# Kernel optimization log

Hardware: AMD Instinct MI355X
Metric: run time of the kernel (lower is better)

Reference implementation:

```python
import jax, jax.numpy as jnp
import numpy as np


def setup_inputs() -> dict:
    key = jax.random.key(0)
    # (B, C, H, W) with H == W, required by the original module's broadcasting.
    x = jax.random.normal(key, (16, 64, 256, 256), dtype=jnp.float32)
    return {"x": x}


def reference(x):
    """Naive real DFT of the original module, computed as a separable contraction.

    Original math (after resolving the meshgrid 'xy' indexing, H == W == N):
      real[b,c,u,v] = sum_{i,j} x[b,c,i,j] * cos(2*pi*(j*u + i*v)/N)
      imag[b,c,u,v] = sum_{i,j} x[b,c,i,j] * sin(-2*pi*(j*u + i*v)/N)
    with u in [0, N/2), v in [0, N/2).
    We use cos(a+b)=cos a cos b - sin a sin b to factorize into matmuls,
    avoiding the (B,C,N,N,N/2,N/2) broadcast intermediate.
    """
    B, C, H, W = x.shape
    assert H == W, "original module's broadcasting requires square input"
    N = H
    K = N // 2
    two_pi = jnp.asarray(2.0 * np.pi, dtype=x.dtype)
    n = jnp.arange(N, dtype=x.dtype) / N          # spatial index / N
    k = jnp.arange(K, dtype=x.dtype)              # frequency index
    ang = two_pi * n[:, None] * k[None, :]        # (N, K)
    Cm = jnp.cos(ang)                             # (N, K)
    Sm = jnp.sin(ang)                             # (N, K)

    # Contract W-axis j against frequency u, then H-axis i against frequency v.
    A = jnp.einsum('bcij,ju->bciu', x, Cm)        # sum_j x * cos(2pi j u / N)
    Bt = jnp.einsum('bcij,ju->bciu', x, Sm)       # sum_j x * sin(2pi j u / N)
    real = jnp.einsum('bciu,iv->bcuv', A, Cm) - jnp.einsum('bciu,iv->bcuv', Bt, Sm)
    imag = -(jnp.einsum('bciu,iv->bcuv', Bt, Cm) + jnp.einsum('bciu,iv->bcuv', A, Sm))
    return real, imag
```

## Files before the change

### kernel.cpp

```cpp
#include <hip/hip_runtime.h>
#include <hip/hip_bf16.h>


typedef __attribute__((ext_vector_type(8))) short short8;
typedef __attribute__((ext_vector_type(4))) short bf16x4;
typedef __attribute__((ext_vector_type(4))) float f32x4;

#define NN 256
#define KF 128
#define NIMG 1024

__device__ __align__(16) short g_Ct[KF * NN];
__device__ __align__(16) short g_St[KF * NN];
__device__ __align__(16) short g_Stn[KF * NN];

__device__ __forceinline__ short f2bf(float f) {
    union { float f; unsigned u; } v; v.f = f;
    unsigned r = v.u + 0x7FFFu + ((v.u >> 16) & 1u);
    return (short)(r >> 16);
}

__global__ void gen_tables() {
    int tid = blockIdx.x * blockDim.x + threadIdx.x;
    if (tid >= KF * NN) return;
    int u = tid >> 8;
    int j = tid & 255;
    int phase = (u * j) & 255;
    float ang = (float)phase * 0.02454369260617026f;
    float s, c;
    sincosf(ang, &s, &c);
    g_Ct[tid]  = f2bf(c);
    g_St[tid]  = f2bf(s);
    g_Stn[tid] = f2bf(-s);
}

#define MFMA(a, b, c) __builtin_amdgcn_mfma_f32_16x16x32_bf16(a, b, c, 0, 0, 0)

__global__ __launch_bounds__(512, 4) void freq_dft(const float* __restrict__ x,
                                                   float* __restrict__ out) {
    __shared__ __align__(16) char lds[65536];

    const int bid = blockIdx.x;
    const int cc  = bid & 7;
    const int q   = bid >> 3;
    const int h   = q & 1;
    const int img = cc + ((q >> 1) << 3);

    const float* __restrict__ X = x + (size_t)img * (NN * NN);
    float* __restrict__ outR = out + (size_t)img * (KF * KF);
    float* __restrict__ outI = outR + (size_t)NIMG * (KF * KF);

    const int lane = threadIdx.x & 63;
    const int wave = threadIdx.x >> 6;
    const int l15  = lane & 15;
    const int lk8  = (lane >> 4) << 3;
    const int lr4  = (lane >> 4) << 2;

    {
        const short* __restrict__ srcC = g_Ct  + h * 64 * NN;
        const short* __restrict__ srcS = g_Stn + h * 64 * NN;
        #pragma unroll
        for (int k = 0; k < 4; ++k) {
            int slot = threadIdx.x + k * 512;
            int row  = slot >> 5;
            int chk  = slot & 31;
            int byte = row * 512 + ((chk << 4) ^ ((row & 7) << 4));
            short8 vC = *(const short8*)(srcC + row * NN + chk * 8);
            short8 vS = *(const short8*)(srcS + row * NN + chk * 8);
            *(short8*)(lds + byte)         = vC;
            *(short8*)(lds + 32768 + byte) = vS;
        }
    }
    __syncthreads();

    f32x4 accA[2][4], accB[2][4];
    {
        const int i0 = wave * 32;
        #pragma unroll
        for (int fi = 0; fi < 2; ++fi)
            #pragma unroll
            for (int fu = 0; fu < 4; ++fu) {
                accA[fi][fu] = (f32x4){0.f, 0.f, 0.f, 0.f};
                accB[fi][fu] = (f32x4){0.f, 0.f, 0.f, 0.f};
            }
        const float* __restrict__ xp0 = X + (i0 + l15) * NN + lk8;
        const float* __restrict__ xp1 = X + (i0 + 16 + l15) * NN + lk8;
        const int wst = wave;
        const int jA  = (wst & 7) * 32;
        const int jB  = ((wst + 1) & 7) * 32;
        f32x4 a0 = *(const f32x4*)(xp0 + jA), a1 = *(const f32x4*)(xp0 + jA + 4);
        f32x4 a2 = *(const f32x4*)(xp1 + jA), a3 = *(const f32x4*)(xp1 + jA + 4);
        f32x4 b0 = *(const f32x4*)(xp0 + jB), b1 = *(const f32x4*)(xp0 + jB + 4);
        f32x4 b2 = *(const f32x4*)(xp1 + jB), b3 = *(const f32x4*)(xp1 + jB + 4);
        #pragma unroll
        for (int t = 0; t < 8; ++t) {
            const int j0 = ((t + wst) & 7) * 32;
            f32x4 c0 = a0, c1 = a1, c2 = a2, c3 = a3;
            a0 = b0; a1 = b1; a2 = b2; a3 = b3;
            if (t < 6) {
                const int jn = ((t + 2 + wst) & 7) * 32;
                b0 = *(const f32x4*)(xp0 + jn); b1 = *(const f32x4*)(xp0 + jn + 4);
                b2 = *(const f32x4*)(xp1 + jn); b3 = *(const f32x4*)(xp1 + jn + 4);
            }
            short8 xb0, xb1;
            xb0[0] = f2bf(c0[0]); xb0[1] = f2bf(c0[1]); xb0[2] = f2bf(c0[2]); xb0[3] = f2bf(c0[3]);
            xb0[4] = f2bf(c1[0]); xb0[5] = f2bf(c1[1]); xb0[6] = f2bf(c1[2]); xb0[7] = f2bf(c1[3]);
            xb1[0] = f2bf(c2[0]); xb1[1] = f2bf(c2[1]); xb1[2] = f2bf(c2[2]); xb1[3] = f2bf(c2[3]);
            xb1[4] = f2bf(c3[0]); xb1[5] = f2bf(c3[1]); xb1[6] = f2bf(c3[2]); xb1[7] = f2bf(c3[3]);
            short8 ca[4], sa[4];
            #pragma unroll
            for (int fu = 0; fu < 4; ++fu) {
                int row  = fu * 16 + l15;
                int byte = row * 512 + (((j0 + lk8) * 2) ^ ((row & 7) << 4));
                ca[fu] = *(const short8*)(lds + byte);
                sa[fu] = *(const short8*)(lds + 32768 + byte);
            }
            #pragma unroll
            for (int fu = 0; fu < 4; ++fu) {
                accA[0][fu] = MFMA(xb0, ca[fu], accA[0][fu]);
                accA[1][fu] = MFMA(xb1, ca[fu], accA[1][fu]);
                accB[0][fu] = MFMA(xb0, sa[fu], accB[0][fu]);
                accB[1][fu] = MFMA(xb1, sa[fu], accB[1][fu]);
            }
        }
    }
    __syncthreads();

    {
        const int i0 = wave * 32;
        #pragma unroll
        for (int fi = 0; fi < 2; ++fi)
            #pragma unroll
            for (int fu = 0; fu < 4; ++fu) {
                int ul    = fu * 16 + l15;
                int ibase = i0 + fi * 16 + lr4;
                int byte  = ul * 512 + ((ibase * 2) ^ ((ul & 7) << 4));
                bf16x4 a4, b4;
                #pragma unroll
                for (int r = 0; r < 4; ++r) {
                    a4[r] = f2bf(accA[fi][fu][r]);
                    b4[r] = f2bf(accB[fi][fu][r]);
                }
                *(bf16x4*)(lds + byte)         = a4;
                *(bf16x4*)(lds + 32768 + byte) = b4;
            }
    }
    __syncthreads();

    {
        const int wu = wave >> 2;
        const int wv = wave & 3;
        const short8 smask = {(short)0x8000, (short)0x8000, (short)0x8000, (short)0x8000,
                              (short)0x8000, (short)0x8000, (short)0x8000, (short)0x8000};
        f32x4 accR[2][2], accI[2][2];
        #pragma unroll
        for (int fu = 0; fu < 2; ++fu)
            #pragma unroll
            for (int fv = 0; fv < 2; ++fv) {
                accR[fu][fv] = (f32x4){0.f, 0.f, 0.f, 0.f};
                accI[fu][fv] = (f32x4){0.f, 0.f, 0.f, 0.f};
            }
        const short* __restrict__ tC0 = g_Ct + (wv * 32 + l15) * NN + lk8;
        const short* __restrict__ tC1 = g_Ct + (wv * 32 + 16 + l15) * NN + lk8;
        const short* __restrict__ tS0 = g_St + (wv * 32 + l15) * NN + lk8;
        const short* __restrict__ tS1 = g_St + (wv * 32 + 16 + l15) * NN + lk8;
        const int wst = wave;
        const int iA  = (wst & 7) * 32;
        const int iB  = ((wst + 1) & 7) * 32;
        short8 ac0 = *(const short8*)(tC0 + iA), ac1 = *(const short8*)(tC1 + iA);
        short8 as0 = *(const short8*)(tS0 + iA), as1 = *(const short8*)(tS1 + iA);
        short8 bc0 = *(const short8*)(tC0 + iB), bc1 = *(const short8*)(tC1 + iB);
        short8 bs0 = *(const short8*)(tS0 + iB), bs1 = *(const short8*)(tS1 + iB);
        #pragma unroll
        for (int t = 0; t < 8; ++t) {
            const int is = ((t + wst) & 7) * 32;
            short8 cb0 = ac0, cb1 = ac1, sb0 = as0, sb1 = as1;
            ac0 = bc0; ac1 = bc1; as0 = bs0; as1 = bs1;
            if (t < 6) {
                const int in = ((t + 2 + wst) & 7) * 32;
                bc0 = *(const short8*)(tC0 + in); bc1 = *(const short8*)(tC1 + in);
                bs0 = *(const short8*)(tS0 + in); bs1 = *(const short8*)(tS1 + in);
            }
            short8 nb0 = sb0 ^ smask;
            short8 nb1 = sb1 ^ smask;
            short8 a[2], bn[2];
            #pragma unroll
            for (int fu = 0; fu < 2; ++fu) {
                int ul   = wu * 32 + fu * 16 + l15;
                int byte = ul * 512 + (((is + lk8) * 2) ^ ((ul & 7) << 4));
                a[fu]  = *(const short8*)(lds + byte);
                bn[fu] = *(const short8*)(lds + 32768 + byte);
            }
            accR[0][0] = MFMA(a[0],  cb0, accR[0][0]);
            accR[1][0] = MFMA(a[1],  cb0, accR[1][0]);
            accR[0][1] = MFMA(a[0],  cb1, accR[0][1]);
            accR[1][1] = MFMA(a[1],  cb1, accR[1][1]);
            accI[0][0] = MFMA(bn[0], cb0, accI[0][0]);
            accI[1][0] = MFMA(bn[1], cb0, accI[1][0]);
            accI[0][1] = MFMA(bn[0], cb1, accI[0][1]);
            accI[1][1] = MFMA(bn[1], cb1, accI[1][1]);
            accR[0][0] = MFMA(bn[0], sb0, accR[0][0]);
            accR[1][0] = MFMA(bn[1], sb0, accR[1][0]);
            accR[0][1] = MFMA(bn[0], sb1, accR[0][1]);
            accR[1][1] = MFMA(bn[1], sb1, accR[1][1]);
            accI[0][0] = MFMA(a[0],  nb0, accI[0][0]);
            accI[1][0] = MFMA(a[1],  nb0, accI[1][0]);
            accI[0][1] = MFMA(a[0],  nb1, accI[0][1]);
            accI[1][1] = MFMA(a[1],  nb1, accI[1][1]);
        }
        #pragma unroll
        for (int fu = 0; fu < 2; ++fu)
            #pragma unroll
            for (int fv = 0; fv < 2; ++fv)
                #pragma unroll
                for (int r = 0; r < 4; ++r) {
                    int u = h * 64 + wu * 32 + fu * 16 + lr4 + r;
                    int v = wv * 32 + fv * 16 + l15;
                    outR[u * KF + v] = accR[fu][fv][r];
                    outI[u * KF + v] = accI[fu][fv][r];
                }
    }
}

extern "C" void kernel_launch(void* const* d_in, const int* in_sizes, int n_in,
                              void* d_out, int out_size, void* d_ws, size_t ws_size,
                              hipStream_t stream) {
    const float* x = (const float*)d_in[0];
    float* out = (float*)d_out;
    gen_tables<<<dim3((KF * NN + 255) / 256), dim3(256), 0, stream>>>();
    freq_dft<<<dim3(NIMG * 2), dim3(512), 0, stream>>>(x, out);
}
```

Measured before the change: 160.7 us.

## Process whole image per block and stream first-stage twiddles from global

Each block now handles one full image instead of half, so the input image is read once rather than twice and the first-stage row transform is no longer duplicated. The first-stage cosine/sine tables are loaded straight from global (L2-resident) into registers with one-step prefetch, instead of being staged through LDS, which drops the initial LDS fill and its barrier. The intermediate needs 128KB of dynamic LDS, so occupancy falls to one block per CU, the launch bound is relaxed, and there is half as many blocks, which risks less latency hiding.

```diff
diff --git a/kernel.cpp b/kernel.cpp
--- a/kernel.cpp
+++ b/kernel.cpp
@@ -36,16 +36,11 @@
 
 #define MFMA(a, b, c) __builtin_amdgcn_mfma_f32_16x16x32_bf16(a, b, c, 0, 0, 0)
 
-__global__ __launch_bounds__(512, 4) void freq_dft(const float* __restrict__ x,
+__global__ __launch_bounds__(512, 2) void freq_dft(const float* __restrict__ x,
                                                    float* __restrict__ out) {
-    __shared__ __align__(16) char lds[65536];
-
-    const int bid = blockIdx.x;
-    const int cc  = bid & 7;
-    const int q   = bid >> 3;
-    const int h   = q & 1;
-    const int img = cc + ((q >> 1) << 3);
-
+    extern __shared__ __align__(16) char lds[];
+
+    const int img = blockIdx.x;
     const float* __restrict__ X = x + (size_t)img * (NN * NN);
     float* __restrict__ outR = out + (size_t)img * (KF * KF);
     float* __restrict__ outI = outR + (size_t)NIMG * (KF * KF);
@@ -55,27 +50,24 @@
     const int l15  = lane & 15;
     const int lk8  = (lane >> 4) << 3;
     const int lr4  = (lane >> 4) << 2;
-
-    {
-        const short* __restrict__ srcC = g_Ct  + h * 64 * NN;
-        const short* __restrict__ srcS = g_Stn + h * 64 * NN;
-        #pragma unroll
-        for (int k = 0; k < 4; ++k) {
-            int slot = threadIdx.x + k * 512;
-            int row  = slot >> 5;
-            int chk  = slot & 31;
-            int byte = row * 512 + ((chk << 4) ^ ((row & 7) << 4));
-            short8 vC = *(const short8*)(srcC + row * NN + chk * 8);
-            short8 vS = *(const short8*)(srcS + row * NN + chk * 8);
-            *(short8*)(lds + byte)         = vC;
-            *(short8*)(lds + 32768 + byte) = vS;
-        }
-    }
-    __syncthreads();
-
-    f32x4 accA[2][4], accB[2][4];
-    {
-        const int i0 = wave * 32;
+    const int wst  = wave;
+
+    const int i0 = wave * 32;
+    const float* __restrict__ xp0 = X + (i0 + l15) * NN + lk8;
+    const float* __restrict__ xp1 = X + (i0 + 16 + l15) * NN + lk8;
+
+    #pragma unroll 1
+    for (int uh = 0; uh < 2; ++uh) {
+        const short* __restrict__ tc0 = g_Ct  + (uh * 64 +  0 + l15) * NN + lk8;
+        const short* __restrict__ tc1 = g_Ct  + (uh * 64 + 16 + l15) * NN + lk8;
+        const short* __restrict__ tc2 = g_Ct  + (uh * 64 + 32 + l15) * NN + lk8;
+        const short* __restrict__ tc3 = g_Ct  + (uh * 64 + 48 + l15) * NN + lk8;
+        const short* __restrict__ ts0 = g_Stn + (uh * 64 +  0 + l15) * NN + lk8;
+        const short* __restrict__ ts1 = g_Stn + (uh * 64 + 16 + l15) * NN + lk8;
+        const short* __restrict__ ts2 = g_Stn + (uh * 64 + 32 + l15) * NN + lk8;
+        const short* __restrict__ ts3 = g_Stn + (uh * 64 + 48 + l15) * NN + lk8;
+
+        f32x4 accA[2][4], accB[2][4];
         #pragma unroll
         for (int fi = 0; fi < 2; ++fi)
             #pragma unroll
@@ -83,18 +75,20 @@
                 accA[fi][fu] = (f32x4){0.f, 0.f, 0.f, 0.f};
                 accB[fi][fu] = (f32x4){0.f, 0.f, 0.f, 0.f};
             }
-        const float* __restrict__ xp0 = X + (i0 + l15) * NN + lk8;
-        const float* __restrict__ xp1 = X + (i0 + 16 + l15) * NN + lk8;
-        const int wst = wave;
-        const int jA  = (wst & 7) * 32;
-        const int jB  = ((wst + 1) & 7) * 32;
+
+        const int jA = (wst & 7) * 32;
+        const int jB = ((wst + 1) & 7) * 32;
         f32x4 a0 = *(const f32x4*)(xp0 + jA), a1 = *(const f32x4*)(xp0 + jA + 4);
         f32x4 a2 = *(const f32x4*)(xp1 + jA), a3 = *(const f32x4*)(xp1 + jA + 4);
         f32x4 b0 = *(const f32x4*)(xp0 + jB), b1 = *(const f32x4*)(xp0 + jB + 4);
         f32x4 b2 = *(const f32x4*)(xp1 + jB), b3 = *(const f32x4*)(xp1 + jB + 4);
+        short8 ca0 = *(const short8*)(tc0 + jA), ca1 = *(const short8*)(tc1 + jA);
+        short8 ca2 = *(const short8*)(tc2 + jA), ca3 = *(const short8*)(tc3 + jA);
+        short8 sa0 = *(const short8*)(ts0 + jA), sa1 = *(const short8*)(ts1 + jA);
+        short8 sa2 = *(const short8*)(ts2 + jA), sa3 = *(const short8*)(ts3 + jA);
+
         #pragma unroll
         for (int t = 0; t < 8; ++t) {
-            const int j0 = ((t + wst) & 7) * 32;
             f32x4 c0 = a0, c1 = a1, c2 = a2, c3 = a3;
             a0 = b0; a1 = b1; a2 = b2; a3 = b3;
             if (t < 6) {
@@ -102,37 +96,40 @@
                 b0 = *(const f32x4*)(xp0 + jn); b1 = *(const f32x4*)(xp0 + jn + 4);
                 b2 = *(const f32x4*)(xp1 + jn); b3 = *(const f32x4*)(xp1 + jn + 4);
             }
+            short8 nc0, nc1, nc2, nc3, ns0, ns1, ns2, ns3;
+            if (t < 7) {
+                const int j1 = ((t + 1 + wst) & 7) * 32;
+                nc0 = *(const short8*)(tc0 + j1); nc1 = *(const short8*)(tc1 + j1);
+                nc2 = *(const short8*)(tc2 + j1); nc3 = *(const short8*)(tc3 + j1);
+                ns0 = *(const short8*)(ts0 + j1); ns1 = *(const short8*)(ts1 + j1);
+                ns2 = *(const short8*)(ts2 + j1); ns3 = *(const short8*)(ts3 + j1);
+            }
             short8 xb0, xb1;
             xb0[0] = f2bf(c0[0]); xb0[1] = f2bf(c0[1]); xb0[2] = f2bf(c0[2]); xb0[3] = f2bf(c0[3]);
             xb0[4] = f2bf(c1[0]); xb0[5] = f2bf(c1[1]); xb0[6] = f2bf(c1[2]); xb0[7] = f2bf(c1[3]);
             xb1[0] = f2bf(c2[0]); xb1[1] = f2bf(c2[1]); xb1[2] = f2bf(c2[2]); xb1[3] = f2bf(c2[3]);
             xb1[4] = f2bf(c3[0]); xb1[5] = f2bf(c3[1]); xb1[6] = f2bf(c3[2]); xb1[7] = f2bf(c3[3]);
-            short8 ca[4], sa[4];
+
+            accA[0][0] = MFMA(xb0, ca0, accA[0][0]); accA[1][0] = MFMA(xb1, ca0, accA[1][0]);
+            accB[0][0] = MFMA(xb0, sa0, accB[0][0]); accB[1][0] = MFMA(xb1, sa0, accB[1][0]);
+            accA[0][1] = MFMA(xb0, ca1, accA[0][1]); accA[1][1] = MFMA(xb1, ca1, accA[1][1]);
+            accB[0][1] = MFMA(xb0, sa1, accB[0][1]); accB[1][1] = MFMA(xb1, sa1, accB[1][1]);
+            accA[0][2] = MFMA(xb0, ca2, accA[0][2]); accA[1][2] = MFMA(xb1, ca2, accA[1][2]);
+            accB[0][2] = MFMA(xb0, sa2, accB[0][2]); accB[1][2] = MFMA(xb1, sa2, accB[1][2]);
+            accA[0][3] = MFMA(xb0, ca3, accA[0][3]); accA[1][3] = MFMA(xb1, ca3, accA[1][3]);
+            accB[0][3] = MFMA(xb0, sa3, accB[0][3]); accB[1][3] = MFMA(xb1, sa3, accB[1][3]);
+
+            if (t < 7) {
+                ca0 = nc0; ca1 = nc1; ca2 = nc2; ca3 = nc3;
+                sa0 = ns0; sa1 = ns1; sa2 = ns2; sa3 = ns3;
+            }
+        }
+
+        #pragma unroll
+        for (int fi = 0; fi < 2; ++fi)
             #pragma unroll
             for (int fu = 0; fu < 4; ++fu) {
-                int row  = fu * 16 + l15;
-                int byte = row * 512 + (((j0 + lk8) * 2) ^ ((row & 7) << 4));
-                ca[fu] = *(const short8*)(lds + byte);
-                sa[fu] = *(const short8*)(lds + 32768 + byte);
-            }
-            #pragma unroll
-            for (int fu = 0; fu < 4; ++fu) {
-                accA[0][fu] = MFMA(xb0, ca[fu], accA[0][fu]);
-                accA[1][fu] = MFMA(xb1, ca[fu], accA[1][fu]);
-                accB[0][fu] = MFMA(xb0, sa[fu], accB[0][fu]);
-                accB[1][fu] = MFMA(xb1, sa[fu], accB[1][fu]);
-            }
-        }
-    }
-    __syncthreads();
-
-    {
-        const int i0 = wave * 32;
-        #pragma unroll
-        for (int fi = 0; fi < 2; ++fi)
-            #pragma unroll
-            for (int fu = 0; fu < 4; ++fu) {
-                int ul    = fu * 16 + l15;
+                int ul    = uh * 64 + fu * 16 + l15;
                 int ibase = i0 + fi * 16 + lr4;
                 int byte  = ul * 512 + ((ibase * 2) ^ ((ul & 7) << 4));
                 bf16x4 a4, b4;
@@ -142,16 +139,22 @@
                     b4[r] = f2bf(accB[fi][fu][r]);
                 }
                 *(bf16x4*)(lds + byte)         = a4;
-                *(bf16x4*)(lds + 32768 + byte) = b4;
+                *(bf16x4*)(lds + 65536 + byte) = b4;
             }
     }
     __syncthreads();
 
-    {
-        const int wu = wave >> 2;
-        const int wv = wave & 3;
-        const short8 smask = {(short)0x8000, (short)0x8000, (short)0x8000, (short)0x8000,
-                              (short)0x8000, (short)0x8000, (short)0x8000, (short)0x8000};
+    const short8 smask = {(short)0x8000, (short)0x8000, (short)0x8000, (short)0x8000,
+                          (short)0x8000, (short)0x8000, (short)0x8000, (short)0x8000};
+    const int vt = wave & 3;
+    const short* __restrict__ tC0 = g_Ct + (vt * 32 +  0 + l15) * NN + lk8;
+    const short* __restrict__ tC1 = g_Ct + (vt * 32 + 16 + l15) * NN + lk8;
+    const short* __restrict__ tS0 = g_St + (vt * 32 +  0 + l15) * NN + lk8;
+    const short* __restrict__ tS1 = g_St + (vt * 32 + 16 + l15) * NN + lk8;
+
+    #pragma unroll 1
+    for (int p = 0; p < 2; ++p) {
+        const int ut = p * 2 + (wave >> 2);
         f32x4 accR[2][2], accI[2][2];
         #pragma unroll
         for (int fu = 0; fu < 2; ++fu)
@@ -160,17 +163,13 @@
                 accR[fu][fv] = (f32x4){0.f, 0.f, 0.f, 0.f};
                 accI[fu][fv] = (f32x4){0.f, 0.f, 0.f, 0.f};
             }
-        const short* __restrict__ tC0 = g_Ct + (wv * 32 + l15) * NN + lk8;
-        const short* __restrict__ tC1 = g_Ct + (wv * 32 + 16 + l15) * NN + lk8;
-        const short* __restrict__ tS0 = g_St + (wv * 32 + l15) * NN + lk8;
-        const short* __restrict__ tS1 = g_St + (wv * 32 + 16 + l15) * NN + lk8;
-        const int wst = wave;
-        const int iA  = (wst & 7) * 32;
-        const int iB  = ((wst + 1) & 7) * 32;
+        const int iA = (wst & 7) * 32;
+        const int iB = ((wst + 1) & 7) * 32;
         short8 ac0 = *(const short8*)(tC0 + iA), ac1 = *(const short8*)(tC1 + iA);
         short8 as0 = *(const short8*)(tS0 + iA), as1 = *(const short8*)(tS1 + iA);
         short8 bc0 = *(const short8*)(tC0 + iB), bc1 = *(const short8*)(tC1 + iB);
         short8 bs0 = *(const short8*)(tS0 + iB), bs1 = *(const short8*)(tS1 + iB);
+
         #pragma unroll
         for (int t = 0; t < 8; ++t) {
             const int is = ((t + wst) & 7) * 32;
@@ -186,10 +185,10 @@
             short8 a[2], bn[2];
             #pragma unroll
             for (int fu = 0; fu < 2; ++fu) {
-                int ul   = wu * 32 + fu * 16 + l15;
+                int ul   = ut * 32 + fu * 16 + l15;
                 int byte = ul * 512 + (((is + lk8) * 2) ^ ((ul & 7) << 4));
                 a[fu]  = *(const short8*)(lds + byte);
-                bn[fu] = *(const short8*)(lds + 32768 + byte);
+                bn[fu] = *(const short8*)(lds + 65536 + byte);
             }
             accR[0][0] = MFMA(a[0],  cb0, accR[0][0]);
             accR[1][0] = MFMA(a[1],  cb0, accR[1][0]);
@@ -214,8 +213,8 @@
             for (int fv = 0; fv < 2; ++fv)
                 #pragma unroll
                 for (int r = 0; r < 4; ++r) {
-                    int u = h * 64 + wu * 32 + fu * 16 + lr4 + r;
-                    int v = wv * 32 + fv * 16 + l15;
+                    int u = ut * 32 + fu * 16 + lr4 + r;
+                    int v = vt * 32 + fv * 16 + l15;
                     outR[u * KF + v] = accR[fu][fv][r];
                     outI[u * KF + v] = accI[fu][fv][r];
                 }
@@ -227,6 +226,8 @@
                               hipStream_t stream) {
     const float* x = (const float*)d_in[0];
     float* out = (float*)d_out;
+    hipFuncSetAttribute((const void*)freq_dft,
+                        hipFuncAttributeMaxDynamicSharedMemorySize, 131072);
     gen_tables<<<dim3((KF * NN + 255) / 256), dim3(256), 0, stream>>>();
-    freq_dft<<<dim3(NIMG * 2), dim3(512), 0, stream>>>(x, out);
-}
+    freq_dft<<<dim3(NIMG), dim3(512), 131072, stream>>>(x, out);
+}
```

After: 226.5 us. 41.0% more time.

## Fold rows i and i+128 into even/odd sums to halve second-stage DFT work

Applied to the files above, without the earlier changes.

The first stage now pairs rows i and i+128 in each wave. Their partial products are combined into sum and difference terms, which serve the even and odd output frequencies because of the period-N symmetry. The second-stage contraction therefore runs over 128 instead of 256 inputs, using new half-size even/odd twiddle tables, and writes adjacent v pairs as float2. Scalar bf16 rounding is also replaced with packed v_cvt_pk_bf16_f32 instructions. The aims are to cut second-stage MFMA and LDS work roughly in half and to reduce conversion ALU cost, at the price of extra tables and slightly different rounding, since the add and subtract happen before the bf16 conversion.

```diff
diff --git a/kernel.cpp b/kernel.cpp
--- a/kernel.cpp
+++ b/kernel.cpp
@@ -5,14 +5,21 @@
 typedef __attribute__((ext_vector_type(8))) short short8;
 typedef __attribute__((ext_vector_type(4))) short bf16x4;
 typedef __attribute__((ext_vector_type(4))) float f32x4;
+typedef __attribute__((ext_vector_type(2))) float f32x2;
+
+typedef union { short8 s8; unsigned u[4]; } pk8;
+typedef union { bf16x4 s4; unsigned u[2]; } pk4;
 
 #define NN 256
 #define KF 128
 #define NIMG 1024
 
 __device__ __align__(16) short g_Ct[KF * NN];
-__device__ __align__(16) short g_St[KF * NN];
 __device__ __align__(16) short g_Stn[KF * NN];
+__device__ __align__(16) short g_T2cE[64 * 128];
+__device__ __align__(16) short g_T2cO[64 * 128];
+__device__ __align__(16) short g_T2sE[64 * 128];
+__device__ __align__(16) short g_T2sO[64 * 128];
 
 __device__ __forceinline__ short f2bf(float f) {
     union { float f; unsigned u; } v; v.f = f;
@@ -20,18 +27,37 @@
     return (short)(r >> 16);
 }
 
+__device__ __forceinline__ unsigned cvtpk(float lo, float hi) {
+    unsigned r;
+    asm("v_cvt_pk_bf16_f32 %0, %1, %2" : "=v"(r) : "v"(lo), "v"(hi));
+    return r;
+}
+
 __global__ void gen_tables() {
     int tid = blockIdx.x * blockDim.x + threadIdx.x;
-    if (tid >= KF * NN) return;
-    int u = tid >> 8;
-    int j = tid & 255;
-    int phase = (u * j) & 255;
-    float ang = (float)phase * 0.02454369260617026f;
-    float s, c;
-    sincosf(ang, &s, &c);
-    g_Ct[tid]  = f2bf(c);
-    g_St[tid]  = f2bf(s);
-    g_Stn[tid] = f2bf(-s);
+    const float w = 0.02454369260617026f;
+    if (tid < KF * NN) {
+        int u = tid >> 8;
+        int j = tid & 255;
+        int phase = (u * j) & 255;
+        float s, c;
+        sincosf((float)phase * w, &s, &c);
+        g_Ct[tid]  = f2bf(c);
+        g_Stn[tid] = f2bf(-s);
+    }
+    if (tid < 64 * 128) {
+        int s = tid >> 7;
+        int i = tid & 127;
+        int pe = (i * (2 * s)) & 255;
+        int po = (i * (2 * s + 1)) & 255;
+        float se, ce, so, co;
+        sincosf((float)pe * w, &se, &ce);
+        sincosf((float)po * w, &so, &co);
+        g_T2cE[tid] = f2bf(ce);
+        g_T2cO[tid] = f2bf(co);
+        g_T2sE[tid] = f2bf(se);
+        g_T2sO[tid] = f2bf(so);
+    }
 }
 
 #define MFMA(a, b, c) __builtin_amdgcn_mfma_f32_16x16x32_bf16(a, b, c, 0, 0, 0)
@@ -55,6 +81,7 @@
     const int l15  = lane & 15;
     const int lk8  = (lane >> 4) << 3;
     const int lr4  = (lane >> 4) << 2;
+    const int wst  = wave;
 
     {
         const short* __restrict__ srcC = g_Ct  + h * 64 * NN;
@@ -75,7 +102,7 @@
 
     f32x4 accA[2][4], accB[2][4];
     {
-        const int i0 = wave * 32;
+        const int i0 = wave * 16;
         #pragma unroll
         for (int fi = 0; fi < 2; ++fi)
             #pragma unroll
@@ -84,10 +111,9 @@
                 accB[fi][fu] = (f32x4){0.f, 0.f, 0.f, 0.f};
             }
         const float* __restrict__ xp0 = X + (i0 + l15) * NN + lk8;
-        const float* __restrict__ xp1 = X + (i0 + 16 + l15) * NN + lk8;
-        const int wst = wave;
-        const int jA  = (wst & 7) * 32;
-        const int jB  = ((wst + 1) & 7) * 32;
+        const float* __restrict__ xp1 = X + (i0 + 128 + l15) * NN + lk8;
+        const int jA = (wst & 7) * 32;
+        const int jB = ((wst + 1) & 7) * 32;
         f32x4 a0 = *(const f32x4*)(xp0 + jA), a1 = *(const f32x4*)(xp0 + jA + 4);
         f32x4 a2 = *(const f32x4*)(xp1 + jA), a3 = *(const f32x4*)(xp1 + jA + 4);
         f32x4 b0 = *(const f32x4*)(xp0 + jB), b1 = *(const f32x4*)(xp0 + jB + 4);
@@ -102,11 +128,13 @@
                 b0 = *(const f32x4*)(xp0 + jn); b1 = *(const f32x4*)(xp0 + jn + 4);
                 b2 = *(const f32x4*)(xp1 + jn); b3 = *(const f32x4*)(xp1 + jn + 4);
             }
-            short8 xb0, xb1;
-            xb0[0] = f2bf(c0[0]); xb0[1] = f2bf(c0[1]); xb0[2] = f2bf(c0[2]); xb0[3] = f2bf(c0[3]);
-            xb0[4] = f2bf(c1[0]); xb0[5] = f2bf(c1[1]); xb0[6] = f2bf(c1[2]); xb0[7] = f2bf(c1[3]);
-            xb1[0] = f2bf(c2[0]); xb1[1] = f2bf(c2[1]); xb1[2] = f2bf(c2[2]); xb1[3] = f2bf(c2[3]);
-            xb1[4] = f2bf(c3[0]); xb1[5] = f2bf(c3[1]); xb1[6] = f2bf(c3[2]); xb1[7] = f2bf(c3[3]);
+            pk8 x0u, x1u;
+            x0u.u[0] = cvtpk(c0[0], c0[1]); x0u.u[1] = cvtpk(c0[2], c0[3]);
+            x0u.u[2] = cvtpk(c1[0], c1[1]); x0u.u[3] = cvtpk(c1[2], c1[3]);
+            x1u.u[0] = cvtpk(c2[0], c2[1]); x1u.u[1] = cvtpk(c2[2], c2[3]);
+            x1u.u[2] = cvtpk(c3[0], c3[1]); x1u.u[3] = cvtpk(c3[2], c3[3]);
+            short8 xb0 = x0u.s8;
+            short8 xb1 = x1u.s8;
             short8 ca[4], sa[4];
             #pragma unroll
             for (int fu = 0; fu < 4; ++fu) {
@@ -127,98 +155,97 @@
     __syncthreads();
 
     {
-        const int i0 = wave * 32;
-        #pragma unroll
-        for (int fi = 0; fi < 2; ++fi)
-            #pragma unroll
-            for (int fu = 0; fu < 4; ++fu) {
-                int ul    = fu * 16 + l15;
-                int ibase = i0 + fi * 16 + lr4;
-                int byte  = ul * 512 + ((ibase * 2) ^ ((ul & 7) << 4));
-                bf16x4 a4, b4;
-                #pragma unroll
-                for (int r = 0; r < 4; ++r) {
-                    a4[r] = f2bf(accA[fi][fu][r]);
-                    b4[r] = f2bf(accB[fi][fu][r]);
-                }
-                *(bf16x4*)(lds + byte)         = a4;
-                *(bf16x4*)(lds + 32768 + byte) = b4;
-            }
+        const int kb = wave * 16 + lr4;
+        #pragma unroll
+        for (int fu = 0; fu < 4; ++fu) {
+            f32x4 eA = accA[0][fu] + accA[1][fu];
+            f32x4 oA = accA[0][fu] - accA[1][fu];
+            f32x4 eB = accB[0][fu] + accB[1][fu];
+            f32x4 oB = accB[0][fu] - accB[1][fu];
+            int ul  = fu * 16 + l15;
+            int sw  = (ul & 7) << 4;
+            int byE = ul * 512 + ((kb * 2) ^ sw);
+            int byO = ul * 512 + (((kb + 128) * 2) ^ sw);
+            pk4 ea, oa, eb, ob;
+            ea.u[0] = cvtpk(eA[0], eA[1]); ea.u[1] = cvtpk(eA[2], eA[3]);
+            oa.u[0] = cvtpk(oA[0], oA[1]); oa.u[1] = cvtpk(oA[2], oA[3]);
+            eb.u[0] = cvtpk(eB[0], eB[1]); eb.u[1] = cvtpk(eB[2], eB[3]);
+            ob.u[0] = cvtpk(oB[0], oB[1]); ob.u[1] = cvtpk(oB[2], oB[3]);
+            *(bf16x4*)(lds + byE)         = ea.s4;
+            *(bf16x4*)(lds + byO)         = oa.s4;
+            *(bf16x4*)(lds + 32768 + byE) = eb.s4;
+            *(bf16x4*)(lds + 32768 + byO) = ob.s4;
+        }
     }
     __syncthreads();
 
     {
         const int wu = wave >> 2;
-        const int wv = wave & 3;
+        const int vt = wave & 3;
         const short8 smask = {(short)0x8000, (short)0x8000, (short)0x8000, (short)0x8000,
                               (short)0x8000, (short)0x8000, (short)0x8000, (short)0x8000};
-        f32x4 accR[2][2], accI[2][2];
+        f32x4 accRE[2], accRO[2], accIE[2], accIO[2];
+        #pragma unroll
+        for (int fu = 0; fu < 2; ++fu) {
+            accRE[fu] = (f32x4){0.f, 0.f, 0.f, 0.f};
+            accRO[fu] = (f32x4){0.f, 0.f, 0.f, 0.f};
+            accIE[fu] = (f32x4){0.f, 0.f, 0.f, 0.f};
+            accIO[fu] = (f32x4){0.f, 0.f, 0.f, 0.f};
+        }
+        const short* __restrict__ pcE = g_T2cE + (vt * 16 + l15) * 128 + lk8;
+        const short* __restrict__ pcO = g_T2cO + (vt * 16 + l15) * 128 + lk8;
+        const short* __restrict__ psE = g_T2sE + (vt * 16 + l15) * 128 + lk8;
+        const short* __restrict__ psO = g_T2sO + (vt * 16 + l15) * 128 + lk8;
+        const int iA = (wst & 3) * 32;
+        const int iB = ((wst + 1) & 3) * 32;
+        short8 AcE = *(const short8*)(pcE + iA), AcO = *(const short8*)(pcO + iA);
+        short8 AsE = *(const short8*)(psE + iA), AsO = *(const short8*)(psO + iA);
+        short8 BcE = *(const short8*)(pcE + iB), BcO = *(const short8*)(pcO + iB);
+        short8 BsE = *(const short8*)(psE + iB), BsO = *(const short8*)(psO + iB);
+        #pragma unroll
+        for (int t = 0; t < 4; ++t) {
+            const int is = ((t + wst) & 3) * 32;
+            short8 cE = AcE, cO = AcO, sE = AsE, sO = AsO;
+            AcE = BcE; AcO = BcO; AsE = BsE; AsO = BsO;
+            if (t < 2) {
+                const int in = ((t + 2 + wst) & 3) * 32;
+                BcE = *(const short8*)(pcE + in); BcO = *(const short8*)(pcO + in);
+                BsE = *(const short8*)(psE + in); BsO = *(const short8*)(psO + in);
+            }
+            short8 sEn = sE ^ smask;
+            short8 sOn = sO ^ smask;
+            short8 eA[2], oA[2], eB[2], oB[2];
+            #pragma unroll
+            for (int fu = 0; fu < 2; ++fu) {
+                int ul  = wu * 32 + fu * 16 + l15;
+                int sw  = (ul & 7) << 4;
+                int byE = ul * 512 + (((is + lk8) * 2) ^ sw);
+                int byO = ul * 512 + (((is + 128 + lk8) * 2) ^ sw);
+                eA[fu] = *(const short8*)(lds + byE);
+                oA[fu] = *(const short8*)(lds + byO);
+                eB[fu] = *(const short8*)(lds + 32768 + byE);
+                oB[fu] = *(const short8*)(lds + 32768 + byO);
+            }
+            accRE[0] = MFMA(eA[0], cE, accRE[0]); accRE[1] = MFMA(eA[1], cE, accRE[1]);
+            accRO[0] = MFMA(oA[0], cO, accRO[0]); accRO[1] = MFMA(oA[1], cO, accRO[1]);
+            accIE[0] = MFMA(eB[0], cE, accIE[0]); accIE[1] = MFMA(eB[1], cE, accIE[1]);
+            accIO[0] = MFMA(oB[0], cO, accIO[0]); accIO[1] = MFMA(oB[1], cO, accIO[1]);
+            accRE[0] = MFMA(eB[0], sE, accRE[0]); accRE[1] = MFMA(eB[1], sE, accRE[1]);
+            accRO[0] = MFMA(oB[0], sO, accRO[0]); accRO[1] = MFMA(oB[1], sO, accRO[1]);
+            accIE[0] = MFMA(eA[0], sEn, accIE[0]); accIE[1] = MFMA(eA[1], sEn, accIE[1]);
+            accIO[0] = MFMA(oA[0], sOn, accIO[0]); accIO[1] = MFMA(oA[1], sOn, accIO[1]);
+        }
         #pragma unroll
         for (int fu = 0; fu < 2; ++fu)
             #pragma unroll
-            for (int fv = 0; fv < 2; ++fv) {
-                accR[fu][fv] = (f32x4){0.f, 0.f, 0.f, 0.f};
-                accI[fu][fv] = (f32x4){0.f, 0.f, 0.f, 0.f};
-            }
-        const short* __restrict__ tC0 = g_Ct + (wv * 32 + l15) * NN + lk8;
-        const short* __restrict__ tC1 = g_Ct + (wv * 32 + 16 + l15) * NN + lk8;
-        const short* __restrict__ tS0 = g_St + (wv * 32 + l15) * NN + lk8;
-        const short* __restrict__ tS1 = g_St + (wv * 32 + 16 + l15) * NN + lk8;
-        const int wst = wave;
-        const int iA  = (wst & 7) * 32;
-        const int iB  = ((wst + 1) & 7) * 32;
-        short8 ac0 = *(const short8*)(tC0 + iA), ac1 = *(const short8*)(tC1 + iA);
-        short8 as0 = *(const short8*)(tS0 + iA), as1 = *(const short8*)(tS1 + iA);
-        short8 bc0 = *(const short8*)(tC0 + iB), bc1 = *(const short8*)(tC1 + iB);
-        short8 bs0 = *(const short8*)(tS0 + iB), bs1 = *(const short8*)(tS1 + iB);
-        #pragma unroll
-        for (int t = 0; t < 8; ++t) {
-            const int is = ((t + wst) & 7) * 32;
-            short8 cb0 = ac0, cb1 = ac1, sb0 = as0, sb1 = as1;
-            ac0 = bc0; ac1 = bc1; as0 = bs0; as1 = bs1;
-            if (t < 6) {
-                const int in = ((t + 2 + wst) & 7) * 32;
-                bc0 = *(const short8*)(tC0 + in); bc1 = *(const short8*)(tC1 + in);
-                bs0 = *(const short8*)(tS0 + in); bs1 = *(const short8*)(tS1 + in);
-            }
-            short8 nb0 = sb0 ^ smask;
-            short8 nb1 = sb1 ^ smask;
-            short8 a[2], bn[2];
-            #pragma unroll
-            for (int fu = 0; fu < 2; ++fu) {
-                int ul   = wu * 32 + fu * 16 + l15;
-                int byte = ul * 512 + (((is + lk8) * 2) ^ ((ul & 7) << 4));
-                a[fu]  = *(const short8*)(lds + byte);
-                bn[fu] = *(const short8*)(lds + 32768 + byte);
-            }
-            accR[0][0] = MFMA(a[0],  cb0, accR[0][0]);
-            accR[1][0] = MFMA(a[1],  cb0, accR[1][0]);
-            accR[0][1] = MFMA(a[0],  cb1, accR[0][1]);
-            accR[1][1] = MFMA(a[1],  cb1, accR[1][1]);
-            accI[0][0] = MFMA(bn[0], cb0, accI[0][0]);
-            accI[1][0] = MFMA(bn[1], cb0, accI[1][0]);
-            accI[0][1] = MFMA(bn[0], cb1, accI[0][1]);
-            accI[1][1] = MFMA(bn[1], cb1, accI[1][1]);
-            accR[0][0] = MFMA(bn[0], sb0, accR[0][0]);
-            accR[1][0] = MFMA(bn[1], sb0, accR[1][0]);
-            accR[0][1] = MFMA(bn[0], sb1, accR[0][1]);
-            accR[1][1] = MFMA(bn[1], sb1, accR[1][1]);
-            accI[0][0] = MFMA(a[0],  nb0, accI[0][0]);
-            accI[1][0] = MFMA(a[1],  nb0, accI[1][0]);
-            accI[0][1] = MFMA(a[0],  nb1, accI[0][1]);
-            accI[1][1] = MFMA(a[1],  nb1, accI[1][1]);
-        }
-        #pragma unroll
-        for (int fu = 0; fu < 2; ++fu)
-            #pragma unroll
-            for (int fv = 0; fv < 2; ++fv)
-                #pragma unroll
-                for (int r = 0; r < 4; ++r) {
-                    int u = h * 64 + wu * 32 + fu * 16 + lr4 + r;
-                    int v = wv * 32 + fv * 16 + l15;
-                    outR[u * KF + v] = accR[fu][fv][r];
-                    outI[u * KF + v] = accI[fu][fv][r];
-                }
+            for (int r = 0; r < 4; ++r) {
+                int u = h * 64 + wu * 32 + fu * 16 + lr4 + r;
+                int v = vt * 32 + 2 * l15;
+                f32x2 vr = {accRE[fu][r], accRO[fu][r]};
+                f32x2 vi = {accIE[fu][r], accIO[fu][r]};
+                *(f32x2*)(outR + u * KF + v) = vr;
+                *(f32x2*)(outI + u * KF + v) = vi;
+            }
     }
 }
 
```

After: 134.5 us. 16.3% less time.
